# Performance work log

Hardware: AMD Instinct MI355X
Metric: run time of the kernel (lower is better)

The kernel has to match this reference:

```python
import jax, jax.numpy as jnp
import numpy as np

MAX_PER_CLASS = 100   # max_num_boxes_per_class
MAX_TOTAL = 300       # max_num_boxes (pad_per_class=False -> output size is MAX_TOTAL)
IOU_THR = 0.5
SCORE_THR = 0.001
NEG = jnp.float32(-1e30)
EPS = 1e-12


def _canon(b):
    # boxes given as any diagonal pair (y1,x1,y2,x2); canonicalize like TF NMS
    ymin = jnp.minimum(b[..., 0], b[..., 2])
    ymax = jnp.maximum(b[..., 0], b[..., 2])
    xmin = jnp.minimum(b[..., 1], b[..., 3])
    xmax = jnp.maximum(b[..., 1], b[..., 3])
    return ymin, xmin, ymax, xmax


def _iou_one_vs_all(box, boxes):
    # box [4], boxes [N,4] -> iou [N]
    y1a, x1a, y2a, x2a = _canon(box)
    y1b, x1b, y2b, x2b = _canon(boxes)
    ih = jnp.maximum(jnp.minimum(y2a, y2b) - jnp.maximum(y1a, y1b), 0.0)
    iw = jnp.maximum(jnp.minimum(x2a, x2b) - jnp.maximum(x1a, x1b), 0.0)
    inter = ih * iw
    area_a = (y2a - y1a) * (x2a - x1a)
    area_b = (y2b - y1b) * (x2b - x1b)
    union = jnp.maximum(area_a + area_b - inter, EPS)
    return inter / union


def _nms_single_class(boxes_c, scores_c):
    # boxes_c [N,4], scores_c [N] -> (scores [K], boxes [K,4], valid [K]) with K=MAX_PER_CLASS
    N = scores_c.shape[0]
    valid = scores_c > SCORE_THR
    s = jnp.where(valid, scores_c, NEG)
    order = jnp.argsort(-s)
    b_sorted = boxes_c[order]          # [N,4]
    s_sorted = s[order]                # [N]
    v_sorted = valid[order]            # [N]

    def step(keep, xs):
        i, box_i, valid_i = xs
        iou_row = _iou_one_vs_all(box_i, b_sorted)          # [N]
        suppressed = jnp.any(keep & (iou_row > IOU_THR))    # vs previously kept only
        keep = keep.at[i].set(valid_i & jnp.logical_not(suppressed))
        return keep, None

    keep0 = jnp.zeros((N,), dtype=bool)
    keep, _ = jax.lax.scan(step, keep0, (jnp.arange(N), b_sorted, v_sorted))

    # cap number of kept boxes at MAX_PER_CLASS (in descending score order)
    rank = jnp.cumsum(keep.astype(jnp.int32)) - 1
    keep = keep & (rank < MAX_PER_CLASS)

    key = jnp.where(keep, s_sorted, NEG)
    top_s, top_i = jax.lax.top_k(key, MAX_PER_CLASS)
    top_boxes = b_sorted[top_i]
    top_valid = top_s > (NEG / 2)
    return top_s, top_boxes, top_valid


def _combined_nms(scores, boxes):
    # scores [B,N,C], boxes [B,N,q,4] with q==1 (boxes shared across classes)
    B, N, C = scores.shape
    q = boxes.shape[2]

    def per_image(scores_i, boxes_i):
        # scores_i [N,C], boxes_i [N,q,4]
        if q == 1:
            cls_boxes = jnp.broadcast_to(boxes_i, (N, C, 4))
        else:
            cls_boxes = boxes_i
        # per-class NMS, vmapped over the class axis
        sc, bx, vd = jax.vmap(_nms_single_class, in_axes=(1, 1))(cls_boxes, scores_i)
        # sc [C,K], bx [C,K,4], vd [C,K]
        cls_ids = jnp.broadcast_to(
            jnp.arange(C, dtype=scores.dtype)[:, None], vd.shape)

        flat_s = jnp.where(vd, sc, NEG).reshape(-1)   # [C*K]
        flat_b = bx.reshape(-1, 4)
        flat_c = cls_ids.reshape(-1)
        flat_v = vd.reshape(-1)

        top_s, idx = jax.lax.top_k(flat_s, MAX_TOTAL)
        out_v = flat_v[idx]
        out_s = jnp.where(out_v, top_s, 0.0)
        out_b = jnp.where(out_v[:, None], flat_b[idx], 0.0)
        out_b = jnp.clip(out_b, 0.0, 1.0)             # clip_boxes=True
        out_c = jnp.where(out_v, flat_c[idx], 0.0)
        count = jnp.sum(out_v.astype(jnp.int32))
        return out_s, out_b, out_c, count

    return jax.vmap(per_image)(scores, boxes)


def setup_inputs() -> dict:
    key = jax.random.key(0)
    k1, k2 = jax.random.split(key)
    B, N, C, Q = 4, 1024, 80, 1
    scores = jax.random.uniform(k1, (B, N, C), dtype=jnp.float32)
    boxes = jax.random.uniform(k2, (B, N, Q, 4), dtype=jnp.float32)
    return {"scores": scores, "boxes": boxes}


def reference(scores, boxes):
    # returns (output_scores, output_boxes, output_classes, valid_counts)
    return _combined_nms(scores, boxes)
```

## Files before the change

### kernel.cpp

```cpp
#include <hip/hip_runtime.h>
#include <stdint.h>

#define N_BOX 1024
#define C_CLS 80
#define B_IMG 4
#define K_PER 100
#define K_TOT 300
#define NEGF  (-1e30f)
#define NCAND (C_CLS * K_PER)
#define M_SEL 8192
#define KPAD  1088

#define OFF_WSCORE  1835008
#define OFF_WSIDX   1963008

typedef unsigned long long u64;
typedef unsigned int u32;

__device__ __forceinline__ int swz(int i) { return i + (i >> 4); }

__device__ __forceinline__ u32 ford(float f) {
    u32 u = __float_as_uint(f);
    return (u & 0x80000000u) ? ~u : (u | 0x80000000u);
}
__device__ __forceinline__ float funord(u32 o) {
    u32 u = (o & 0x80000000u) ? (o ^ 0x80000000u) : ~o;
    return __uint_as_float(u);
}

__device__ __forceinline__ bool iou_gt(float4 a, float aa, float4 b, float ab) {
#pragma clang fp contract(off)
    float ih = fminf(a.z, b.z) - fmaxf(a.x, b.x); ih = fmaxf(ih, 0.0f);
    float iw = fminf(a.w, b.w) - fmaxf(a.y, b.y); iw = fmaxf(iw, 0.0f);
    float inter = ih * iw;
    float uni = fmaxf(aa + ab - inter, 1e-12f);
    return (inter / uni) > 0.5f;
}

__global__ __launch_bounds__(256, 2) void nms_classes(
        const float* __restrict__ scores,
        const float* __restrict__ boxes,
        float* __restrict__ ws_score,
        int*   __restrict__ ws_idx)
{
    __shared__ u64    key[KPAD];
    __shared__ float4 bx[N_BOX];
    __shared__ float  ar[N_BOX];
    __shared__ float4 wb[2][64];
    __shared__ float  wa[2][64];
    __shared__ float4 kb[128];
    __shared__ float  ka[128];
    __shared__ int    kept_t[K_PER];
    __shared__ u32    colk16[4][64];
    __shared__ u64    sup64[4];
    __shared__ int    sh_nvalid, sh_kept;

    const int tid  = threadIdx.x;
    const int lane = tid & 63;
    const int b  = blockIdx.x / C_CLS;
    const int c  = blockIdx.x % C_CLS;

    if (tid == 0) { sh_nvalid = 0; sh_kept = 0; }

    for (int n = tid; n < N_BOX; n += 256) {
        float4 v = ((const float4*)boxes)[b * N_BOX + n];
        {
#pragma clang fp contract(off)
            float y1 = fminf(v.x, v.z), y2 = fmaxf(v.x, v.z);
            float x1 = fminf(v.y, v.w), x2 = fmaxf(v.y, v.w);
            bx[n] = make_float4(y1, x1, y2, x2);
            ar[n] = (y2 - y1) * (x2 - x1);
        }
    }
    __syncthreads();

    u64 r[4];
    {
        const float* sc = scores + (size_t)(b * N_BOX) * C_CLS + c;
        int lv = 0;
        #pragma unroll
        for (int q = 0; q < 4; ++q) {
            int v = tid * 4 + q;
            float s0 = sc[(size_t)v * C_CLS];
            bool valid = s0 > 0.001f;
            float s = valid ? s0 : NEGF;
            r[q] = ((u64)ford(s) << 32) | (u32)(N_BOX - 1 - v);
            lv += valid ? 1 : 0;
        }
        if (lv) atomicAdd(&sh_nvalid, lv);
    }

    #define CE(a, b, d) { u64 _mx = (a) > (b) ? (a) : (b); \
                          u64 _mn = (a) > (b) ? (b) : (a); \
                          (a) = (d) ? _mx : _mn; (b) = (d) ? _mn : _mx; }
    CE(r[0], r[1], true); CE(r[2], r[3], false);

    for (int k = 4; k <= N_BOX; k <<= 1) {
        const bool d = ((tid & (k >> 2)) == 0);
        for (int j = k >> 1; j > 0; j >>= 1) {
            if (j >= 256) {
                __syncthreads();
                #pragma unroll
                for (int q = 0; q < 4; ++q) key[swz(tid * 4 + q)] = r[q];
                __syncthreads();
                const bool upper = ((tid * 4) & j) != 0;
                #pragma unroll
                for (int q = 0; q < 4; ++q) {
                    u64 pv = key[swz((tid * 4 + q) ^ j)];
                    u64 mx = r[q] > pv ? r[q] : pv;
                    u64 mn = r[q] > pv ? pv : r[q];
                    r[q] = (d != upper) ? mx : mn;
                }
            } else if (j >= 4) {
                const int dl = j >> 2;
                const bool upper = (lane & dl) != 0;
                #pragma unroll
                for (int q = 0; q < 4; ++q) {
                    u64 pv = __shfl_xor(r[q], dl);
                    u64 mx = r[q] > pv ? r[q] : pv;
                    u64 mn = r[q] > pv ? pv : r[q];
                    r[q] = (d != upper) ? mx : mn;
                }
            } else if (j == 2) {
                CE(r[0], r[2], d); CE(r[1], r[3], d);
            } else {
                CE(r[0], r[1], d); CE(r[2], r[3], d);
            }
        }
    }
    #undef CE

    __syncthreads();
    #pragma unroll
    for (int q = 0; q < 4; ++q) key[swz(tid * 4 + q)] = r[q];
    __syncthreads();

    if (tid < 64) {
        u64 kv = key[swz(tid)];
        int idx = (N_BOX - 1) - (int)(u32)(kv & 0xFFFFFFFFu);
        wb[0][tid] = bx[idx];
        wa[0][tid] = ar[idx];
    }

    const int nvalid = sh_nvalid;
    const int nwin = (nvalid + 63) >> 6;
    const int me  = tid & 63;
    const int grp = tid >> 6;

    for (int w = 0; w < nwin; ++w) {
        const int cur = w & 1;
        __syncthreads();
        if (sh_kept >= K_PER) break;
        const int kept0 = sh_kept;
        const int bt = w * 64;

        if (grp == 1 && (w + 1) < nwin) {
            u64 kv = key[swz((bt + 64 + me) & (N_BOX - 1))];
            int idx = (N_BOX - 1) - (int)(u32)(kv & 0xFFFFFFFFu);
            wb[cur ^ 1][me] = bx[idx];
            wa[cur ^ 1][me] = ar[idx];
        }

        const float4 qm = wb[cur][me];
        const float  am = wa[cur][me];

        {
            float4 wrow[16]; float warow[16];
            #pragma unroll
            for (int rq = 0; rq < 16; ++rq) {
                wrow[rq]  = wb[cur][grp * 16 + rq];
                warow[rq] = wa[cur][grp * 16 + rq];
            }
            u32 bits = 0;
            #pragma unroll
            for (int rq = 0; rq < 16; ++rq) {
                int rr = grp * 16 + rq;
                bool kill = (rr != me) && iou_gt(wrow[rq], warow[rq], qm, am);
                bits |= ((u32)kill) << rq;
            }
            colk16[grp][me] = bits;
        }

        {
            bool supme = false;
            for (int t0 = 0; grp + 4 * t0 < kept0; t0 += 8) {
                float4 kbl[8]; float kal[8];
                #pragma unroll
                for (int i = 0; i < 8; ++i) {
                    int k = grp + 4 * (t0 + i);
                    kbl[i] = kb[k]; kal[i] = ka[k];
                }
                #pragma unroll
                for (int i = 0; i < 8; ++i) {
                    int k = grp + 4 * (t0 + i);
                    if (k < kept0 && iou_gt(kbl[i], kal[i], qm, am)) supme = true;
                }
            }
            u64 bal = __ballot(supme);
            if (lane == 0) sup64[grp] = bal;
        }
        __syncthreads();

        if (grp == 0) {
            u32 c0 = colk16[0][lane], c1 = colk16[1][lane];
            u32 c2 = colk16[2][lane], c3 = colk16[3][lane];
            u64 colkill = (u64)c0 | ((u64)c1 << 16)
                        | ((u64)c2 << 32) | ((u64)c3 << 48);
            u64 supp = sup64[0] | sup64[1] | sup64[2] | sup64[3];
            bool in = ((bt + lane) < nvalid) && !((supp >> lane) & 1ull);
            u64 pending = __ballot(in);
            int kept = kept0;
            while (pending && kept < K_PER) {
                int t0 = __ffsll((long long)pending) - 1;
                if (lane == 0) kept_t[kept] = bt + t0;
                if (lane == t0) { kb[kept] = qm; ka[kept] = am; }
                kept++;
                bool kill = (colkill >> t0) & 1ull;
                pending &= ~(1ull << t0);
                pending &= ~__ballot(kill);
            }
            if (lane == 0) sh_kept = kept;
        }
    }
    __syncthreads();

    const int kept = sh_kept;
    if (tid < K_PER) {
        int ob = (b * C_CLS + c) * K_PER + tid;
        if (tid < kept) {
            u64 k = key[swz(kept_t[tid])];
            ws_score[ob] = funord((u32)(k >> 32));
            ws_idx[ob]   = (N_BOX - 1) - (int)(u32)(k & 0xFFFFFFFFu);
        } else {
            ws_score[ob] = NEGF;
            ws_idx[ob]   = 0;
        }
    }
}

__global__ __launch_bounds__(1024) void final_topk(
        const float* __restrict__ ws_score,
        const int*   __restrict__ ws_idx,
        const float* __restrict__ boxes,
        float* __restrict__ out)
{
    __shared__ u32 skey[NCAND];
    __shared__ u32 hist4[256 * 4];
    __shared__ u64 list[512];
    __shared__ int sh_sel;
    __shared__ u32 sh_need;
    __shared__ int sh_cnt, sh_valid;

    const int tid = threadIdx.x;
    const int b = blockIdx.x;
    const int base = b * NCAND;

    if (tid == 0) { sh_cnt = 0; sh_valid = 0; }
    for (int i = tid; i < NCAND; i += 1024)
        skey[i] = ford(ws_score[base + i]);
    if (tid < 512) list[tid] = 0;
    hist4[tid] = 0;
    __syncthreads();

    u64 prefix = 0;
    u32 need = K_TOT;
    const int rounds[6] = {7, 6, 5, 4, 1, 0};
    const int slot = tid & 3;

    for (int rd = 0; rd < 6; ++rd) {
        const int d = rounds[rd];
        for (int i = tid; i < NCAND; i += 1024) {
            u64 k = ((u64)skey[i] << 32) | (u32)(M_SEL - 1 - i);
            bool match = (d == 7) || (((k ^ prefix) >> (8 * (d + 1))) == 0);
            if (match)
                atomicAdd(&hist4[(((u32)(k >> (8 * d)) & 0xFFu) << 2) | slot], 1u);
        }
        __syncthreads();
        if (tid < 64) {
            const int l = tid;
            u32 h[4];
            #pragma unroll
            for (int q = 0; q < 4; ++q) {
                int bin = 4 * l + q;
                h[q] = hist4[bin * 4 + 0] + hist4[bin * 4 + 1]
                     + hist4[bin * 4 + 2] + hist4[bin * 4 + 3];
                hist4[bin * 4 + 0] = 0; hist4[bin * 4 + 1] = 0;
                hist4[bin * 4 + 2] = 0; hist4[bin * 4 + 3] = 0;
            }
            u32 s3 = h[3], s2 = h[2] + s3, s1 = h[1] + s2, s0 = h[0] + s1;
            u32 tot = s0, S = tot;
            #pragma unroll
            for (int off = 1; off < 64; off <<= 1) {
                u32 t = __shfl(S, (l + off) & 63);
                if (l + off < 64) S += t;
            }
            u32 T = S - tot;
            u32 sv0 = s0 + T, sv1 = s1 + T, sv2 = s2 + T, sv3 = s3 + T;
            if (sv0 >= need && sv1 < need) { sh_sel = 4*l;     sh_need = need - sv1; }
            if (sv1 >= need && sv2 < need) { sh_sel = 4*l + 1; sh_need = need - sv2; }
            if (sv2 >= need && sv3 < need) { sh_sel = 4*l + 2; sh_need = need - sv3; }
            if (sv3 >= need && T   < need) { sh_sel = 4*l + 3; sh_need = need - T;   }
        }
        __syncthreads();
        prefix |= ((u64)(u32)sh_sel) << (8 * d);
        need = sh_need;
        __syncthreads();
    }

    for (int i = tid; i < NCAND; i += 1024) {
        u64 k = ((u64)skey[i] << 32) | (u32)(M_SEL - 1 - i);
        if (k >= prefix) {
            int p = atomicAdd(&sh_cnt, 1);
            if (p < 512) list[p] = k;
        }
    }
    __syncthreads();

    if (tid < 64) {
        const int l = tid;
        u64 e[8];
        #pragma unroll
        for (int q = 0; q < 8; ++q) e[q] = list[l * 8 + q];
        #define CE2(a, b, dd) { u64 _mx = (a) > (b) ? (a) : (b); \
                                u64 _mn = (a) > (b) ? (b) : (a); \
                                (a) = (dd) ? _mx : _mn; (b) = (dd) ? _mn : _mx; }
        CE2(e[0], e[1], true);  CE2(e[2], e[3], false);
        CE2(e[4], e[5], true);  CE2(e[6], e[7], false);
        CE2(e[0], e[2], true);  CE2(e[1], e[3], true);
        CE2(e[4], e[6], false); CE2(e[5], e[7], false);
        CE2(e[0], e[1], true);  CE2(e[2], e[3], true);
        CE2(e[4], e[5], false); CE2(e[6], e[7], false);
        for (int k = 8; k <= 512; k <<= 1) {
            const bool d = ((l & (k >> 3)) == 0);
            for (int j = k >> 1; j >= 8; j >>= 1) {
                const int dl = j >> 3;
                const bool upper = (l & dl) != 0;
                #pragma unroll
                for (int q = 0; q < 8; ++q) {
                    u64 pv = __shfl_xor(e[q], dl);
                    u64 mx = e[q] > pv ? e[q] : pv;
                    u64 mn = e[q] > pv ? pv : e[q];
                    e[q] = (d != upper) ? mx : mn;
                }
            }
            CE2(e[0], e[4], d); CE2(e[1], e[5], d);
            CE2(e[2], e[6], d); CE2(e[3], e[7], d);
            CE2(e[0], e[2], d); CE2(e[1], e[3], d);
            CE2(e[4], e[6], d); CE2(e[5], e[7], d);
            CE2(e[0], e[1], d); CE2(e[2], e[3], d);
            CE2(e[4], e[5], d); CE2(e[6], e[7], d);
        }
        #undef CE2
        #pragma unroll
        for (int q = 0; q < 8; ++q) list[l * 8 + q] = e[q];
    }
    __syncthreads();

    float* out_s = out;
    float* out_b = out + B_IMG * K_TOT;
    float* out_c = out + B_IMG * K_TOT * 5;
    float* out_n = out + B_IMG * K_TOT * 6;

    for (int i = tid; i < K_TOT; i += 1024) {
        u64 k = list[i];
        float s = funord((u32)(k >> 32));
        int flat = (M_SEL - 1) - (int)(u32)(k & 0xFFFFFFFFu);
        bool valid = s > (-5e29f);
        float os = 0.0f, oc = 0.0f;
        float4 ob = make_float4(0.0f, 0.0f, 0.0f, 0.0f);
        if (valid && flat < NCAND) {
            int cc = flat / K_PER;
            int n  = ws_idx[base + flat];
            float4 bb = ((const float4*)boxes)[b * N_BOX + n];
            os = s;
            oc = (float)cc;
            ob.x = fminf(fmaxf(bb.x, 0.0f), 1.0f);
            ob.y = fminf(fmaxf(bb.y, 0.0f), 1.0f);
            ob.z = fminf(fmaxf(bb.z, 0.0f), 1.0f);
            ob.w = fminf(fmaxf(bb.w, 0.0f), 1.0f);
            atomicAdd(&sh_valid, 1);
        }
        out_s[b * K_TOT + i] = os;
        ((float4*)out_b)[b * K_TOT + i] = ob;
        out_c[b * K_TOT + i] = oc;
    }
    __syncthreads();
    if (tid == 0) out_n[b] = (float)sh_valid;
}

extern "C" void kernel_launch(void* const* d_in, const int* in_sizes, int n_in,
                              void* d_out, int out_size, void* d_ws, size_t ws_size,
                              hipStream_t stream) {
    const float* scores = (const float*)d_in[0];
    const float* boxes  = (const float*)d_in[1];

    char* ws = (char*)d_ws;
    float* ws_score = (float*)(ws + OFF_WSCORE);
    int*   ws_idx   = (int*)  (ws + OFF_WSIDX);

    nms_classes<<<dim3(B_IMG * C_CLS), dim3(256), 0, stream>>>(
        scores, boxes, ws_score, ws_idx);
    final_topk<<<dim3(B_IMG), dim3(1024), 0, stream>>>(
        ws_score, ws_idx, boxes, (float*)d_out);
}
```

Measured before the change: 117.0 us.

## Fuse final top-k into NMS kernel via last-block-done counter, add fast IoU test

Merges the second final_topk kernel into nms_classes: each block atomically increments a per-image done counter, and the last block for that image runs the radix top-k with 256 threads, reusing aliased shared memory. This removes one kernel launch and the gap between the two kernels. A memset of the counters is added before the launch. The IoU test now compares 2*inter against union with a tolerance band and only falls back to the exact division in ambiguous cases. The greedy keep loop records kept boxes in a bitmask and writes them out in parallel afterwards, instead of writing inside the serial loop. The cost is that the tail top-k runs on a single 256-thread block per image, and the hipMemsetAsync adds an operation of its own.

```diff
diff --git a/kernel.cpp b/kernel.cpp
--- a/kernel.cpp
+++ b/kernel.cpp
@@ -11,6 +11,7 @@
 #define M_SEL 8192
 #define KPAD  1088
 
+#define OFF_DONE    0
 #define OFF_WSCORE  1835008
 #define OFF_WSIDX   1963008
 
@@ -28,32 +29,42 @@
     return __uint_as_float(u);
 }
 
-__device__ __forceinline__ bool iou_gt(float4 a, float aa, float4 b, float ab) {
+__device__ __forceinline__ bool iou_gt_fast(float4 a, float aa, float4 b, float ab) {
 #pragma clang fp contract(off)
     float ih = fminf(a.z, b.z) - fmaxf(a.x, b.x); ih = fmaxf(ih, 0.0f);
     float iw = fminf(a.w, b.w) - fmaxf(a.y, b.y); iw = fmaxf(iw, 0.0f);
     float inter = ih * iw;
     float uni = fmaxf(aa + ab - inter, 1e-12f);
-    return (inter / uni) > 0.5f;
+    float diff = 2.0f * inter - uni;
+    bool kill = diff > uni * 2.4e-7f;
+    if (__builtin_expect(!kill && diff > 0.0f, 0))
+        kill = (inter / uni) > 0.5f;
+    return kill;
 }
 
 __global__ __launch_bounds__(256, 2) void nms_classes(
         const float* __restrict__ scores,
         const float* __restrict__ boxes,
         float* __restrict__ ws_score,
-        int*   __restrict__ ws_idx)
+        int*   __restrict__ ws_idx,
+        float* __restrict__ out,
+        int*   __restrict__ done_cnt)
 {
-    __shared__ u64    key[KPAD];
-    __shared__ float4 bx[N_BOX];
-    __shared__ float  ar[N_BOX];
-    __shared__ float4 wb[2][64];
-    __shared__ float  wa[2][64];
-    __shared__ float4 kb[128];
-    __shared__ float  ka[128];
+    __shared__ __align__(16) char smraw[40192];
+    u64*    key  = (u64*)(smraw);
+    float4* bx   = (float4*)(smraw + 8704);
+    float*  ar   = (float*)(smraw + 25088);
+    float4* wbuf = (float4*)(smraw + 29184);
+    float*  wab  = (float*)(smraw + 31232);
+    float4* kb   = (float4*)(smraw + 31744);
+    float*  ka   = (float*)(smraw + 33792);
+
     __shared__ int    kept_t[K_PER];
     __shared__ u32    colk16[4][64];
     __shared__ u64    sup64[4];
-    __shared__ int    sh_nvalid, sh_kept;
+    __shared__ int    sh_nvalid, sh_kept, sh_rank;
+    __shared__ int    sh_sel, sh_cnt, sh_valid;
+    __shared__ u32    sh_need;
 
     const int tid  = threadIdx.x;
     const int lane = tid & 63;
@@ -138,8 +149,8 @@
     if (tid < 64) {
         u64 kv = key[swz(tid)];
         int idx = (N_BOX - 1) - (int)(u32)(kv & 0xFFFFFFFFu);
-        wb[0][tid] = bx[idx];
-        wa[0][tid] = ar[idx];
+        wbuf[tid] = bx[idx];
+        wab[tid]  = ar[idx];
     }
 
     const int nvalid = sh_nvalid;
@@ -157,25 +168,25 @@
         if (grp == 1 && (w + 1) < nwin) {
             u64 kv = key[swz((bt + 64 + me) & (N_BOX - 1))];
             int idx = (N_BOX - 1) - (int)(u32)(kv & 0xFFFFFFFFu);
-            wb[cur ^ 1][me] = bx[idx];
-            wa[cur ^ 1][me] = ar[idx];
-        }
-
-        const float4 qm = wb[cur][me];
-        const float  am = wa[cur][me];
+            wbuf[(cur ^ 1) * 64 + me] = bx[idx];
+            wab[(cur ^ 1) * 64 + me]  = ar[idx];
+        }
+
+        const float4 qm = wbuf[cur * 64 + me];
+        const float  am = wab[cur * 64 + me];
 
         {
             float4 wrow[16]; float warow[16];
             #pragma unroll
             for (int rq = 0; rq < 16; ++rq) {
-                wrow[rq]  = wb[cur][grp * 16 + rq];
-                warow[rq] = wa[cur][grp * 16 + rq];
+                wrow[rq]  = wbuf[cur * 64 + grp * 16 + rq];
+                warow[rq] = wab[cur * 64 + grp * 16 + rq];
             }
             u32 bits = 0;
             #pragma unroll
             for (int rq = 0; rq < 16; ++rq) {
                 int rr = grp * 16 + rq;
-                bool kill = (rr != me) && iou_gt(wrow[rq], warow[rq], qm, am);
+                bool kill = (rr != me) && iou_gt_fast(wrow[rq], warow[rq], qm, am);
                 bits |= ((u32)kill) << rq;
             }
             colk16[grp][me] = bits;
@@ -193,7 +204,7 @@
                 #pragma unroll
                 for (int i = 0; i < 8; ++i) {
                     int k = grp + 4 * (t0 + i);
-                    if (k < kept0 && iou_gt(kbl[i], kal[i], qm, am)) supme = true;
+                    if (k < kept0 && iou_gt_fast(kbl[i], kal[i], qm, am)) supme = true;
                 }
             }
             u64 bal = __ballot(supme);
@@ -210,14 +221,19 @@
             bool in = ((bt + lane) < nvalid) && !((supp >> lane) & 1ull);
             u64 pending = __ballot(in);
             int kept = kept0;
+            u64 acc = 0;
             while (pending && kept < K_PER) {
                 int t0 = __ffsll((long long)pending) - 1;
-                if (lane == 0) kept_t[kept] = bt + t0;
-                if (lane == t0) { kb[kept] = qm; ka[kept] = am; }
+                acc |= 1ull << t0;
                 kept++;
                 bool kill = (colkill >> t0) & 1ull;
                 pending &= ~(1ull << t0);
                 pending &= ~__ballot(kill);
+            }
+            if ((acc >> lane) & 1ull) {
+                int pos = kept0 + (int)__popcll(acc & ((1ull << lane) - 1ull));
+                kept_t[pos] = bt + lane;
+                kb[pos] = qm; ka[pos] = am;
             }
             if (lane == 0) sh_kept = kept;
         }
@@ -236,30 +252,26 @@
             ws_idx[ob]   = 0;
         }
     }
-}
-
-__global__ __launch_bounds__(1024) void final_topk(
-        const float* __restrict__ ws_score,
-        const int*   __restrict__ ws_idx,
-        const float* __restrict__ boxes,
-        float* __restrict__ out)
-{
-    __shared__ u32 skey[NCAND];
-    __shared__ u32 hist4[256 * 4];
-    __shared__ u64 list[512];
-    __shared__ int sh_sel;
-    __shared__ u32 sh_need;
-    __shared__ int sh_cnt, sh_valid;
-
-    const int tid = threadIdx.x;
-    const int b = blockIdx.x;
-    const int base = b * NCAND;
-
+
+    __syncthreads();
+    if (tid == 0) {
+        __threadfence();
+        sh_rank = atomicAdd(&done_cnt[b], 1);
+    }
+    __syncthreads();
+    if (sh_rank != C_CLS - 1) return;
+    __threadfence();
+
+    u32* skey  = (u32*)(smraw);
+    u32* hist4 = (u32*)(smraw + 32000);
+    u64* list  = (u64*)(smraw + 36096);
+
+    const int base2 = b * NCAND;
     if (tid == 0) { sh_cnt = 0; sh_valid = 0; }
-    for (int i = tid; i < NCAND; i += 1024)
-        skey[i] = ford(ws_score[base + i]);
-    if (tid < 512) list[tid] = 0;
-    hist4[tid] = 0;
+    for (int i = tid; i < NCAND; i += 256)
+        skey[i] = ford(ws_score[base2 + i]);
+    for (int i = tid; i < 512; i += 256) list[i] = 0;
+    for (int i = tid; i < 1024; i += 256) hist4[i] = 0;
     __syncthreads();
 
     u64 prefix = 0;
@@ -269,7 +281,7 @@
 
     for (int rd = 0; rd < 6; ++rd) {
         const int d = rounds[rd];
-        for (int i = tid; i < NCAND; i += 1024) {
+        for (int i = tid; i < NCAND; i += 256) {
             u64 k = ((u64)skey[i] << 32) | (u32)(M_SEL - 1 - i);
             bool match = (d == 7) || (((k ^ prefix) >> (8 * (d + 1))) == 0);
             if (match)
@@ -307,7 +319,7 @@
         __syncthreads();
     }
 
-    for (int i = tid; i < NCAND; i += 1024) {
+    for (int i = tid; i < NCAND; i += 256) {
         u64 k = ((u64)skey[i] << 32) | (u32)(M_SEL - 1 - i);
         if (k >= prefix) {
             int p = atomicAdd(&sh_cnt, 1);
@@ -361,27 +373,27 @@
     float* out_c = out + B_IMG * K_TOT * 5;
     float* out_n = out + B_IMG * K_TOT * 6;
 
-    for (int i = tid; i < K_TOT; i += 1024) {
+    for (int i = tid; i < K_TOT; i += 256) {
         u64 k = list[i];
         float s = funord((u32)(k >> 32));
         int flat = (M_SEL - 1) - (int)(u32)(k & 0xFFFFFFFFu);
         bool valid = s > (-5e29f);
         float os = 0.0f, oc = 0.0f;
-        float4 ob = make_float4(0.0f, 0.0f, 0.0f, 0.0f);
+        float4 obv = make_float4(0.0f, 0.0f, 0.0f, 0.0f);
         if (valid && flat < NCAND) {
             int cc = flat / K_PER;
-            int n  = ws_idx[base + flat];
+            int n  = ws_idx[base2 + flat];
             float4 bb = ((const float4*)boxes)[b * N_BOX + n];
             os = s;
             oc = (float)cc;
-            ob.x = fminf(fmaxf(bb.x, 0.0f), 1.0f);
-            ob.y = fminf(fmaxf(bb.y, 0.0f), 1.0f);
-            ob.z = fminf(fmaxf(bb.z, 0.0f), 1.0f);
-            ob.w = fminf(fmaxf(bb.w, 0.0f), 1.0f);
+            obv.x = fminf(fmaxf(bb.x, 0.0f), 1.0f);
+            obv.y = fminf(fmaxf(bb.y, 0.0f), 1.0f);
+            obv.z = fminf(fmaxf(bb.z, 0.0f), 1.0f);
+            obv.w = fminf(fmaxf(bb.w, 0.0f), 1.0f);
             atomicAdd(&sh_valid, 1);
         }
         out_s[b * K_TOT + i] = os;
-        ((float4*)out_b)[b * K_TOT + i] = ob;
+        ((float4*)out_b)[b * K_TOT + i] = obv;
         out_c[b * K_TOT + i] = oc;
     }
     __syncthreads();
@@ -395,11 +407,11 @@
     const float* boxes  = (const float*)d_in[1];
 
     char* ws = (char*)d_ws;
+    int*   done_cnt = (int*)(ws + OFF_DONE);
     float* ws_score = (float*)(ws + OFF_WSCORE);
     int*   ws_idx   = (int*)  (ws + OFF_WSIDX);
 
+    hipMemsetAsync(done_cnt, 0, B_IMG * sizeof(int), stream);
     nms_classes<<<dim3(B_IMG * C_CLS), dim3(256), 0, stream>>>(
-        scores, boxes, ws_score, ws_idx);
-    final_topk<<<dim3(B_IMG), dim3(1024), 0, stream>>>(
-        ws_score, ws_idx, boxes, (float*)d_out);
+        scores, boxes, ws_score, ws_idx, (float*)d_out, done_cnt);
 }
```

Result: slower. 127.3 us (+8.8%).
